# Kernel tuning notes

Hardware: AMD Instinct MI355X
Metric: run time of the kernel (lower is better)

The kernel has to match this reference:

```python
import jax, jax.numpy as jnp
import numpy as np

B, L, H = 1024, 256, 128
NUM_TEAMS, NUM_VENUES, NUM_RESULTS = 1000, 3, 3
OUT_IN = 4 * H + 2 + 3  # past_repr (4H+2) concat stats (3)


def setup_inputs() -> dict:
    key = jax.random.key(0)
    ks = jax.random.split(key, 16)
    return {
        "team_embed": jax.random.normal(ks[0], (NUM_TEAMS, H), jnp.float32) * 0.02,
        "venue_embed": jax.random.normal(ks[1], (NUM_VENUES, H), jnp.float32) * 0.02,
        "result_embed": jax.random.normal(ks[2], (NUM_RESULTS, H), jnp.float32) * 0.02,
        "W_out": jax.random.normal(ks[3], (OUT_IN, NUM_RESULTS), jnp.float32) * 0.02,
        "b_out": jnp.zeros((NUM_RESULTS,), jnp.float32),
        "goals_for": jax.random.uniform(ks[4], (B, L), jnp.float32) * 5.0,
        "goals_against": jax.random.uniform(ks[5], (B, L), jnp.float32) * 5.0,
        "stats": jax.random.uniform(ks[6], (B, 3), jnp.float32),
        "venue": jax.random.randint(ks[7], (B, L), 0, NUM_VENUES),
        "team": jax.random.randint(ks[8], (B, L), 0, NUM_TEAMS),
        "opponent": jax.random.randint(ks[9], (B, L), 0, NUM_TEAMS),
        "result": jax.random.randint(ks[10], (B, L), 0, NUM_RESULTS),
        "next_venue": jax.random.randint(ks[11], (B,), 0, NUM_VENUES),
        "next_team": jax.random.randint(ks[12], (B,), 0, NUM_TEAMS),
        "next_opponent": jax.random.randint(ks[13], (B,), 0, NUM_TEAMS),
    }


def reference(team_embed, venue_embed, result_embed, W_out, b_out,
              goals_for, goals_against, stats,
              venue, team, opponent, result,
              next_venue, next_team, next_opponent):
    h = team_embed.shape[1]
    # (B, L, 4H+2): embedding gathers + goal scalars concatenated
    past_seq = jnp.concatenate([
        venue_embed[venue], team_embed[team], team_embed[opponent],
        result_embed[result], goals_for[..., None], goals_against[..., None],
    ], axis=-1)
    # (B, 3H): next-match condition vector
    next_cond = jnp.concatenate([
        venue_embed[next_venue], team_embed[next_team], team_embed[next_opponent],
    ], axis=-1)
    scale = jnp.asarray(3 * h, past_seq.dtype) ** 0.5
    scores = jnp.einsum('bld,bd->bl', past_seq[..., : 3 * h], next_cond) / scale
    attn = jax.nn.softmax(scores, axis=1)                 # over L
    past_repr = jnp.einsum('bl,bld->bd', attn, past_seq)  # (B, 4H+2)
    logits = jnp.concatenate([past_repr, stats], axis=-1) @ W_out + b_out
    return logits
```

## Files before the change

### kernel.cpp

```cpp
#include <hip/hip_runtime.h>

#define L_ 256
#define H_ 128

#define KSCALE 0.07362222315f

template <int CTRL>
__device__ __forceinline__ float dpp_add(float v) {
    return v + __int_as_float(__builtin_amdgcn_update_dpp(
        0, __float_as_int(v), CTRL, 0xF, 0xF, true));
}

__device__ __forceinline__ float dppReduce16(float v) {
    v = dpp_add<0xB1>(v);
    v = dpp_add<0x4E>(v);
    v = dpp_add<0x141>(v);
    v = dpp_add<0x140>(v);
    return v;
}

__device__ __forceinline__ float dppReduce64(float v) {
    v = dppReduce16(v);
    v = dpp_add<0x142>(v);
    v = dpp_add<0x143>(v);
    return v;
}

__global__ __launch_bounds__(256) void fused_match_kernel(
    const float* __restrict__ team_embed,
    const float* __restrict__ venue_embed,
    const float* __restrict__ result_embed,
    const float* __restrict__ W_out,
    const float* __restrict__ b_out,
    const float* __restrict__ goals_for,
    const float* __restrict__ goals_against,
    const float* __restrict__ stats,
    const int* __restrict__ venue,
    const int* __restrict__ team,
    const int* __restrict__ opponent,
    const int* __restrict__ result,
    const int* __restrict__ next_venue,
    const int* __restrict__ next_team,
    const int* __restrict__ next_opponent,
    float* __restrict__ out)
{
    const int b    = blockIdx.x;
    const int t    = threadIdx.x;
    const int lane = t & 63;
    const int wid  = t >> 6;
    const int grp  = lane >> 4;
    const int ci   = lane & 15;

    __shared__ float  nc[384];
    __shared__ int    s_team[L_];
    __shared__ int    s_opp[L_];
    __shared__ int    s_venue[L_];
    __shared__ float  s_e[L_];
    __shared__ float  s_dotv[3];
    __shared__ float4 s_accT[16][32];
    __shared__ float4 s_accO[16][32];
    __shared__ float  s_redw[4][7];
    __shared__ float  s_pr[517];

    const int base = b * L_;
    const int my_venue  = venue[base + t];
    const int my_result = result[base + t];
    const float my_gf   = goals_for[base + t];
    const float my_ga   = goals_against[base + t];
    s_team[t]  = team[base + t];
    s_opp[t]   = opponent[base + t];
    s_venue[t] = my_venue;

    const int nv  = next_venue[b];
    const int ntm = next_team[b];
    const int nop = next_opponent[b];
    if (t < 128) {
        nc[t]       = venue_embed[nv * H_ + t];
        nc[128 + t] = team_embed[ntm * H_ + t];
    } else {
        nc[128 + t] = team_embed[nop * H_ + (t - 128)];
    }
    __syncthreads();

    if (wid < 3) {
        float a = venue_embed[wid * H_ + lane]      * nc[lane]
                + venue_embed[wid * H_ + 64 + lane] * nc[64 + lane];
        a = dppReduce64(a);
        if (lane == 63) s_dotv[wid] = a;
    }
    __syncthreads();

    const float4 nct0 = ((const float4*)(nc + 128))[ci];
    const float4 nct1 = ((const float4*)(nc + 128))[ci + 16];
    const float4 nco0 = ((const float4*)(nc + 256))[ci];
    const float4 nco1 = ((const float4*)(nc + 256))[ci + 16];

    const float4* te4 = (const float4*)team_embed;
    const int lb = wid * 64;

    float4 accT0 = make_float4(0.f, 0.f, 0.f, 0.f);
    float4 accT1 = make_float4(0.f, 0.f, 0.f, 0.f);
    float4 accO0 = make_float4(0.f, 0.f, 0.f, 0.f);
    float4 accO1 = make_float4(0.f, 0.f, 0.f, 0.f);

    {
        const int l0 = lb + grp;
        const int iT = s_team[l0] * 32;
        const int iO = s_opp[l0]  * 32;
        float4 vT0 = te4[iT + ci];
        float4 vT1 = te4[iT + 16 + ci];
        float4 vO0 = te4[iO + ci];
        float4 vO1 = te4[iO + 16 + ci];
        float  dv  = s_dotv[s_venue[l0]];

        #pragma unroll 4
        for (int i = 0; i < 16; ++i) {
            const float4 cT0 = vT0, cT1 = vT1, cO0 = vO0, cO1 = vO1;
            const float  cdv = dv;
            const int    cl  = lb + i * 4 + grp;
            if (i < 15) {
                const int ln = cl + 4;
                const int jT = s_team[ln] * 32;
                const int jO = s_opp[ln]  * 32;
                vT0 = te4[jT + ci];
                vT1 = te4[jT + 16 + ci];
                vO0 = te4[jO + ci];
                vO1 = te4[jO + 16 + ci];
                dv  = s_dotv[s_venue[ln]];
            }
            float p0 = cT0.x * nct0.x + cT0.y * nct0.y + cT0.z * nct0.z + cT0.w * nct0.w;
            float p1 = cT1.x * nct1.x + cT1.y * nct1.y + cT1.z * nct1.z + cT1.w * nct1.w;
            float p2 = cO0.x * nco0.x + cO0.y * nco0.y + cO0.z * nco0.z + cO0.w * nco0.w;
            float p3 = cO1.x * nco1.x + cO1.y * nco1.y + cO1.z * nco1.z + cO1.w * nco1.w;
            float p  = (p0 + p1) + (p2 + p3);
            p = dppReduce16(p);
            const float e = exp2f((p + cdv) * KSCALE);
            if (ci == 0) s_e[cl] = e;
            accT0.x += e * cT0.x; accT0.y += e * cT0.y; accT0.z += e * cT0.z; accT0.w += e * cT0.w;
            accT1.x += e * cT1.x; accT1.y += e * cT1.y; accT1.z += e * cT1.z; accT1.w += e * cT1.w;
            accO0.x += e * cO0.x; accO0.y += e * cO0.y; accO0.z += e * cO0.z; accO0.w += e * cO0.w;
            accO1.x += e * cO1.x; accO1.y += e * cO1.y; accO1.z += e * cO1.z; accO1.w += e * cO1.w;
        }
    }
    {
        const int hs = wid * 4 + grp;
        s_accT[hs][ci]      = accT0;
        s_accT[hs][ci + 16] = accT1;
        s_accO[hs][ci]      = accO0;
        s_accO[hs][ci + 16] = accO1;
    }
    __syncthreads();

    {
        const float e = s_e[t];
        float vals[7];
        vals[0] = e;
        vals[1] = (my_venue  == 0) ? e : 0.f;
        vals[2] = (my_venue  == 1) ? e : 0.f;
        vals[3] = (my_result == 0) ? e : 0.f;
        vals[4] = (my_result == 1) ? e : 0.f;
        vals[5] = e * my_gf;
        vals[6] = e * my_ga;
        #pragma unroll
        for (int k = 0; k < 7; ++k) vals[k] = dppReduce64(vals[k]);
        if (lane == 63) {
            #pragma unroll
            for (int k = 0; k < 7; ++k) s_redw[wid][k] = vals[k];
        }
    }
    __syncthreads();

    #define RW(k) (s_redw[0][k] + s_redw[1][k] + s_redw[2][k] + s_redw[3][k])

    if (t < 64) {
        const int seg = t >> 5;
        const int cc  = t & 31;
        float4 a = make_float4(0.f, 0.f, 0.f, 0.f);
        #pragma unroll
        for (int h = 0; h < 16; ++h) {
            const float4 v = seg ? s_accO[h][cc] : s_accT[h][cc];
            a.x += v.x; a.y += v.y; a.z += v.z; a.w += v.w;
        }
        const float invZ = 1.f / RW(0);
        const int d = 128 + seg * 128 + cc * 4;
        s_pr[d + 0] = a.x * invZ;
        s_pr[d + 1] = a.y * invZ;
        s_pr[d + 2] = a.z * invZ;
        s_pr[d + 3] = a.w * invZ;
        if (t < 2) s_pr[512 + t] = RW(5 + t) * invZ;
        if (t >= 2 && t < 5) s_pr[512 + t] = stats[b * 3 + t - 2];
    } else if (t < 192) {
        const int j = t - 64;
        const float invZ = 1.f / RW(0);
        const float w0 = RW(1) * invZ;
        const float w1 = RW(2) * invZ;
        const float w2 = 1.f - w0 - w1;
        s_pr[j] = w0 * venue_embed[j] + w1 * venue_embed[H_ + j]
                + w2 * venue_embed[2 * H_ + j];
    } else {
        const int j = t - 192;
        const float invZ = 1.f / RW(0);
        const float w3 = RW(3) * invZ;
        const float w4 = RW(4) * invZ;
        const float w5 = 1.f - w3 - w4;
        s_pr[384 + j] = w3 * result_embed[j]      + w4 * result_embed[H_ + j]
                      + w5 * result_embed[2 * H_ + j];
        s_pr[448 + j] = w3 * result_embed[64 + j] + w4 * result_embed[H_ + 64 + j]
                      + w5 * result_embed[2 * H_ + 64 + j];
    }
    #undef RW
    __syncthreads();

    if (wid < 3) {
        float acc = 0.f;
        for (int d = lane; d < 517; d += 64) acc += s_pr[d] * W_out[d * 3 + wid];
        acc = dppReduce64(acc);
        if (lane == 63) out[b * 3 + wid] = acc + b_out[wid];
    }
}

extern "C" void kernel_launch(void* const* d_in, const int* in_sizes, int n_in,
                              void* d_out, int out_size, void* d_ws, size_t ws_size,
                              hipStream_t stream) {
    const float* team_embed    = (const float*)d_in[0];
    const float* venue_embed   = (const float*)d_in[1];
    const float* result_embed  = (const float*)d_in[2];
    const float* W_out         = (const float*)d_in[3];
    const float* b_out         = (const float*)d_in[4];
    const float* goals_for     = (const float*)d_in[5];
    const float* goals_against = (const float*)d_in[6];
    const float* stats         = (const float*)d_in[7];
    const int* venue           = (const int*)d_in[8];
    const int* team            = (const int*)d_in[9];
    const int* opponent        = (const int*)d_in[10];
    const int* result          = (const int*)d_in[11];
    const int* next_venue      = (const int*)d_in[12];
    const int* next_team       = (const int*)d_in[13];
    const int* next_opponent   = (const int*)d_in[14];
    float* out = (float*)d_out;

    const int B = in_sizes[12];
    fused_match_kernel<<<B, 256, 0, stream>>>(
        team_embed, venue_embed, result_embed, W_out, b_out,
        goals_for, goals_against, stats,
        venue, team, opponent, result,
        next_venue, next_team, next_opponent, out);
}
```

Before: 104.6 us.

## Double block size to 512 threads with 32-lane per-row gather and reduce

Moves the per-batch block from 256 to 512 threads. Each half-wave of 32 lanes now handles one history row with one float4 of team and one of opponent per lane, where previously a 16-lane group handled two of each. The dot-product reduction changes to a 32-lane DPP plus ds_swizzle, and the tail work is spread across more threads. The aim is more gather loads in flight and lower per-thread register pressure, at the cost of idle threads in the serial phases and a larger block per CU.

New measurement: 106.1 us. Within noise of the previous version (+1.4%).

```diff
diff --git a/kernel.cpp b/kernel.cpp
--- a/kernel.cpp
+++ b/kernel.cpp
@@ -19,6 +19,12 @@
     return v;
 }
 
+__device__ __forceinline__ float reduce32(float v) {
+    v = dppReduce16(v);
+    v += __int_as_float(__builtin_amdgcn_ds_swizzle(__float_as_int(v), 0x401F));
+    return v;
+}
+
 __device__ __forceinline__ float dppReduce64(float v) {
     v = dppReduce16(v);
     v = dpp_add<0x142>(v);
@@ -26,7 +32,7 @@
     return v;
 }
 
-__global__ __launch_bounds__(256) void fused_match_kernel(
+__global__ __launch_bounds__(512, 8) void fused_match_kernel(
     const float* __restrict__ team_embed,
     const float* __restrict__ venue_embed,
     const float* __restrict__ result_embed,
@@ -48,8 +54,9 @@
     const int t    = threadIdx.x;
     const int lane = t & 63;
     const int wid  = t >> 6;
-    const int grp  = lane >> 4;
-    const int ci   = lane & 15;
+    const int half = lane >> 5;
+    const int c    = lane & 31;
+    const int gh   = t >> 5;
 
     __shared__ float  nc[384];
     __shared__ int    s_team[L_];
@@ -63,23 +70,24 @@
     __shared__ float  s_pr[517];
 
     const int base = b * L_;
-    const int my_venue  = venue[base + t];
-    const int my_result = result[base + t];
-    const float my_gf   = goals_for[base + t];
-    const float my_ga   = goals_against[base + t];
-    s_team[t]  = team[base + t];
-    s_opp[t]   = opponent[base + t];
-    s_venue[t] = my_venue;
+    int   my_venue = 0, my_result = 0;
+    float my_gf = 0.f, my_ga = 0.f;
+    if (t < L_) {
+        my_venue  = venue[base + t];
+        my_result = result[base + t];
+        my_gf     = goals_for[base + t];
+        my_ga     = goals_against[base + t];
+        s_team[t]  = team[base + t];
+        s_opp[t]   = opponent[base + t];
+        s_venue[t] = my_venue;
+    }
 
     const int nv  = next_venue[b];
     const int ntm = next_team[b];
     const int nop = next_opponent[b];
-    if (t < 128) {
-        nc[t]       = venue_embed[nv * H_ + t];
-        nc[128 + t] = team_embed[ntm * H_ + t];
-    } else {
-        nc[128 + t] = team_embed[nop * H_ + (t - 128)];
-    }
+    if (t < 128)      nc[t] = venue_embed[nv * H_ + t];
+    else if (t < 256) nc[t] = team_embed[ntm * H_ + (t - 128)];
+    else if (t < 384) nc[t] = team_embed[nop * H_ + (t - 256)];
     __syncthreads();
 
     if (wid < 3) {
@@ -90,68 +98,43 @@
     }
     __syncthreads();
 
-    const float4 nct0 = ((const float4*)(nc + 128))[ci];
-    const float4 nct1 = ((const float4*)(nc + 128))[ci + 16];
-    const float4 nco0 = ((const float4*)(nc + 256))[ci];
-    const float4 nco1 = ((const float4*)(nc + 256))[ci + 16];
-
+    const float4 nct_c = ((const float4*)(nc + 128))[c];
+    const float4 nco_c = ((const float4*)(nc + 256))[c];
     const float4* te4 = (const float4*)team_embed;
-    const int lb = wid * 64;
-
-    float4 accT0 = make_float4(0.f, 0.f, 0.f, 0.f);
-    float4 accT1 = make_float4(0.f, 0.f, 0.f, 0.f);
-    float4 accO0 = make_float4(0.f, 0.f, 0.f, 0.f);
-    float4 accO1 = make_float4(0.f, 0.f, 0.f, 0.f);
-
+    const int lb = wid * 32 + half;
+
+    float4 accT = make_float4(0.f, 0.f, 0.f, 0.f);
+    float4 accO = make_float4(0.f, 0.f, 0.f, 0.f);
     {
-        const int l0 = lb + grp;
-        const int iT = s_team[l0] * 32;
-        const int iO = s_opp[l0]  * 32;
-        float4 vT0 = te4[iT + ci];
-        float4 vT1 = te4[iT + 16 + ci];
-        float4 vO0 = te4[iO + ci];
-        float4 vO1 = te4[iO + 16 + ci];
-        float  dv  = s_dotv[s_venue[l0]];
+        float4 vT = te4[s_team[lb] * 32 + c];
+        float4 vO = te4[s_opp[lb]  * 32 + c];
+        float  dv = s_dotv[s_venue[lb]];
 
         #pragma unroll 4
         for (int i = 0; i < 16; ++i) {
-            const float4 cT0 = vT0, cT1 = vT1, cO0 = vO0, cO1 = vO1;
+            const float4 cT = vT, cO = vO;
             const float  cdv = dv;
-            const int    cl  = lb + i * 4 + grp;
+            const int    cl  = lb + 2 * i;
             if (i < 15) {
-                const int ln = cl + 4;
-                const int jT = s_team[ln] * 32;
-                const int jO = s_opp[ln]  * 32;
-                vT0 = te4[jT + ci];
-                vT1 = te4[jT + 16 + ci];
-                vO0 = te4[jO + ci];
-                vO1 = te4[jO + 16 + ci];
-                dv  = s_dotv[s_venue[ln]];
+                const int ln = cl + 2;
+                vT = te4[s_team[ln] * 32 + c];
+                vO = te4[s_opp[ln]  * 32 + c];
+                dv = s_dotv[s_venue[ln]];
             }
-            float p0 = cT0.x * nct0.x + cT0.y * nct0.y + cT0.z * nct0.z + cT0.w * nct0.w;
-            float p1 = cT1.x * nct1.x + cT1.y * nct1.y + cT1.z * nct1.z + cT1.w * nct1.w;
-            float p2 = cO0.x * nco0.x + cO0.y * nco0.y + cO0.z * nco0.z + cO0.w * nco0.w;
-            float p3 = cO1.x * nco1.x + cO1.y * nco1.y + cO1.z * nco1.z + cO1.w * nco1.w;
-            float p  = (p0 + p1) + (p2 + p3);
-            p = dppReduce16(p);
+            float p = cT.x * nct_c.x + cT.y * nct_c.y + cT.z * nct_c.z + cT.w * nct_c.w
+                    + cO.x * nco_c.x + cO.y * nco_c.y + cO.z * nco_c.z + cO.w * nco_c.w;
+            p = reduce32(p);
             const float e = exp2f((p + cdv) * KSCALE);
-            if (ci == 0) s_e[cl] = e;
-            accT0.x += e * cT0.x; accT0.y += e * cT0.y; accT0.z += e * cT0.z; accT0.w += e * cT0.w;
-            accT1.x += e * cT1.x; accT1.y += e * cT1.y; accT1.z += e * cT1.z; accT1.w += e * cT1.w;
-            accO0.x += e * cO0.x; accO0.y += e * cO0.y; accO0.z += e * cO0.z; accO0.w += e * cO0.w;
-            accO1.x += e * cO1.x; accO1.y += e * cO1.y; accO1.z += e * cO1.z; accO1.w += e * cO1.w;
+            if (c == 0) s_e[cl] = e;
+            accT.x += e * cT.x; accT.y += e * cT.y; accT.z += e * cT.z; accT.w += e * cT.w;
+            accO.x += e * cO.x; accO.y += e * cO.y; accO.z += e * cO.z; accO.w += e * cO.w;
         }
     }
-    {
-        const int hs = wid * 4 + grp;
-        s_accT[hs][ci]      = accT0;
-        s_accT[hs][ci + 16] = accT1;
-        s_accO[hs][ci]      = accO0;
-        s_accO[hs][ci + 16] = accO1;
-    }
-    __syncthreads();
-
-    {
+    s_accT[gh][c] = accT;
+    s_accO[gh][c] = accO;
+    __syncthreads();
+
+    if (t < L_) {
         const float e = s_e[t];
         float vals[7];
         vals[0] = e;
@@ -175,10 +158,11 @@
     if (t < 64) {
         const int seg = t >> 5;
         const int cc  = t & 31;
+        const float4 (*acc)[32] = seg ? s_accO : s_accT;
         float4 a = make_float4(0.f, 0.f, 0.f, 0.f);
         #pragma unroll
         for (int h = 0; h < 16; ++h) {
-            const float4 v = seg ? s_accO[h][cc] : s_accT[h][cc];
+            const float4 v = acc[h][cc];
             a.x += v.x; a.y += v.y; a.z += v.z; a.w += v.w;
         }
         const float invZ = 1.f / RW(0);
@@ -187,8 +171,6 @@
         s_pr[d + 1] = a.y * invZ;
         s_pr[d + 2] = a.z * invZ;
         s_pr[d + 3] = a.w * invZ;
-        if (t < 2) s_pr[512 + t] = RW(5 + t) * invZ;
-        if (t >= 2 && t < 5) s_pr[512 + t] = stats[b * 3 + t - 2];
     } else if (t < 192) {
         const int j = t - 64;
         const float invZ = 1.f / RW(0);
@@ -197,16 +179,18 @@
         const float w2 = 1.f - w0 - w1;
         s_pr[j] = w0 * venue_embed[j] + w1 * venue_embed[H_ + j]
                 + w2 * venue_embed[2 * H_ + j];
-    } else {
+    } else if (t < 320) {
         const int j = t - 192;
         const float invZ = 1.f / RW(0);
         const float w3 = RW(3) * invZ;
         const float w4 = RW(4) * invZ;
         const float w5 = 1.f - w3 - w4;
-        s_pr[384 + j] = w3 * result_embed[j]      + w4 * result_embed[H_ + j]
+        s_pr[384 + j] = w3 * result_embed[j] + w4 * result_embed[H_ + j]
                       + w5 * result_embed[2 * H_ + j];
-        s_pr[448 + j] = w3 * result_embed[64 + j] + w4 * result_embed[H_ + 64 + j]
-                      + w5 * result_embed[2 * H_ + 64 + j];
+    } else if (t < 322) {
+        s_pr[512 + (t - 320)] = RW(5 + (t - 320)) / RW(0);
+    } else if (t < 325) {
+        s_pr[514 + (t - 322)] = stats[b * 3 + (t - 322)];
     }
     #undef RW
     __syncthreads();
@@ -240,7 +224,7 @@
     float* out = (float*)d_out;
 
     const int B = in_sizes[12];
-    fused_match_kernel<<<B, 256, 0, stream>>>(
+    fused_match_kernel<<<B, 512, 0, stream>>>(
         team_embed, venue_embed, result_embed, W_out, b_out,
         goals_for, goals_against, stats,
         venue, team, opponent, result,
```
